# Optimization experiments

Hardware: AMD Instinct MI355X
Metric: run time of the kernel (lower is better)

The kernel has to match this reference:

```python
import jax, jax.numpy as jnp
import numpy as np

B, H, TQ, TK, DH = 4, 8, 128, 128, 64
N_MEM, D_MEM, TOPK, HID = 100000, 512, 32, 128


def setup_inputs() -> dict:
    key = jax.random.key(0)
    ks = jax.random.split(key, 12)
    return {
        "q": jax.random.normal(ks[0], (B, H, TQ, DH), jnp.float32),
        "k_ctx": jax.random.normal(ks[1], (B, H, TK, DH), jnp.float32),
        "v_ctx": jax.random.normal(ks[2], (B, H, TK, DH), jnp.float32),
        "q_for_mem": jax.random.normal(ks[3], (B, TQ, D_MEM), jnp.float32),
        "mem_keys": jax.random.normal(ks[4], (N_MEM, D_MEM), jnp.float32),
        "mem_values": jax.random.normal(ks[5], (N_MEM, D_MEM), jnp.float32),
        "Wk": jax.random.normal(ks[6], (DH, D_MEM), jnp.float32) / np.sqrt(D_MEM),
        "Wv": jax.random.normal(ks[7], (DH, D_MEM), jnp.float32) / np.sqrt(D_MEM),
        "W1": jax.random.normal(ks[8], (HID, 2 * DH), jnp.float32) / np.sqrt(2 * DH),
        "b1": jnp.zeros((HID,), jnp.float32),
        "w2": jax.random.normal(ks[9], (HID,), jnp.float32) / np.sqrt(HID),
        "b2": jnp.zeros((1,), jnp.float32),
    }


def reference(q, k_ctx, v_ctx, q_for_mem, mem_keys, mem_values, Wk, Wv, W1, b1, w2, b2):
    # --- MemoryBank.retrieve: dense scores + top-k gather ---
    mem_scores = jnp.einsum('btd,nd->btn', q_for_mem, mem_keys)          # [B,TQ,N]
    _, idx = jax.lax.top_k(mem_scores, TOPK)                             # [B,TQ,K]
    K_mem = mem_keys[idx] @ Wk.T                                         # [B,TQ,K,DH] (mem_k_proj)
    V_mem = mem_values[idx] @ Wv.T                                       # [B,TQ,K,DH] (mem_v_proj)

    # --- ParametricScoreMLP: f([q;k]) = w2 . relu(W1q q + W1k k + b1) + b2 ---
    W1q, W1k = W1[:, :DH], W1[:, DH:]                                    # split concat linear
    q_part = jnp.einsum('bhtd,ed->bhte', q, W1q)                         # [B,H,TQ,HID]
    kctx_part = jnp.einsum('bhsd,ed->bhse', k_ctx, W1k)                  # [B,H,TK,HID]
    kmem_part = jnp.einsum('btkd,ed->btke', K_mem, W1k)                  # [B,TQ,K,HID]

    h_ctx = jax.nn.relu(q_part[:, :, :, None, :] + kctx_part[:, :, None, :, :] + b1)
    s_ctx = jnp.einsum('bhtse,e->bhts', h_ctx, w2) + b2[0]               # [B,H,TQ,TK]
    h_mem = jax.nn.relu(q_part[:, :, :, None, :] + kmem_part[:, None, :, :, :] + b1)
    s_mem = jnp.einsum('bhtke,e->bhtk', h_mem, w2) + b2[0]               # [B,H,TQ,K]

    scores = jnp.concatenate([s_ctx, s_mem], axis=-1)                    # [B,H,TQ,TK+K]
    weights = jax.nn.softmax(scores, axis=-1)

    w_ctx, w_mem = weights[..., :TK], weights[..., TK:]
    out = jnp.einsum('bhts,bhsd->bhtd', w_ctx, v_ctx) \
        + jnp.einsum('bhtk,btkd->bhtd', w_mem, V_mem)                    # [B,H,TQ,DH]
    return out, weights
```

## Files before the change

kernel.cpp:

```cpp
#include <hip/hip_runtime.h>
#include <cmath>

constexpr int B_ = 4, H_ = 8, TQ_ = 128, TK_ = 128, DH_ = 64;
constexpr int NMEM = 100000, DM = 512, TOPK = 32, HID = 128;
constexpr int R_ = B_ * TQ_;
constexpr int CTILE = 128, RTILE = 64;
constexpr int NCHP = 784;
constexpr int NPAD = NCHP * CTILE;
constexpr int KC = 16;
constexpr int NCAND = NCHP * KC;
constexpr int KSEL = 48;
constexpr int CAP  = 128;
constexpr int NLD  = NCAND / 256;

using f32x4  = __attribute__((ext_vector_type(4))) float;
using bf16x8 = __attribute__((ext_vector_type(8))) short;
using u16x8  = __attribute__((ext_vector_type(8))) unsigned short;

#define GLOAD16(g, l) __builtin_amdgcn_global_load_lds( \
    (const __attribute__((address_space(1))) void*)(g), \
    (__attribute__((address_space(3))) void*)(l), 16, 0, 0)

static __device__ __forceinline__ unsigned short f2bf(float f) {
    unsigned u = __float_as_uint(f);
    u = (u + 0x7FFFu + ((u >> 16) & 1u)) >> 16;
    return (unsigned short)u;
}

__global__ __launch_bounds__(256)
void k0_cvt(const float* __restrict__ mk, const float* __restrict__ qm,
            unsigned short* __restrict__ dst)
{
    const long totalmk = (long)NPAD * DM;
    const long nvalid  = (long)NMEM * DM;
    const long total   = totalmk + (long)R_ * DM;
    long stride = (long)gridDim.x * 256 * 8;
    for (long base = ((long)blockIdx.x * 256 + threadIdx.x) * 8; base < total; base += stride) {
        u16x8 o;
        const float* src = nullptr;
        long off = 0;
        if (base < totalmk) {
            if (base < nvalid) { src = mk; off = base; }
        } else { src = qm; off = base - totalmk; }
        if (src) {
            float4 v0 = *reinterpret_cast<const float4*>(src + off);
            float4 v1 = *reinterpret_cast<const float4*>(src + off + 4);
            o[0] = f2bf(v0.x); o[1] = f2bf(v0.y); o[2] = f2bf(v0.z); o[3] = f2bf(v0.w);
            o[4] = f2bf(v1.x); o[5] = f2bf(v1.y); o[6] = f2bf(v1.z); o[7] = f2bf(v1.w);
        } else {
            o = (u16x8)0;
        }
        *reinterpret_cast<u16x8*>(dst + base) = o;
    }
}

__global__ __launch_bounds__(256)
void k1_mfma(const unsigned short* __restrict__ qmb, const unsigned short* __restrict__ mkb,
             unsigned* __restrict__ cand_k, int* __restrict__ cand_i)
{
    const int wgid = blockIdx.x;
    const int xcd = wgid & 7;
    const int k9 = wgid >> 3;
    const int chunk = xcd * 98 + (k9 >> 3);
    const int rt = k9 & 7;
    const int row0 = rt * RTILE;
    const int col0 = chunk * CTILE;
    const int tid = threadIdx.x;
    const int lane = tid & 63, w = tid >> 6;
    const int wm = w >> 1, wn = w & 1;

    __shared__ __align__(16) char smem[64 * 132 * 4];
    char* Abase = smem;
    char* Bbase = smem + 8192;
    float* scf = (float*)smem;

    const char* srcA[2];
    const char* srcB[4];
#pragma unroll
    for (int p = 0; p < 2; ++p) {
        int X = p * 4096 + w * 1024 + lane * 16;
        int r = X >> 7, c = (X & 127) ^ ((r & 7) << 4);
        srcA[p] = (const char*)qmb + (size_t)(row0 + r) * 1024 + c;
    }
#pragma unroll
    for (int p = 0; p < 4; ++p) {
        int X = p * 4096 + w * 1024 + lane * 16;
        int r = X >> 7, c = (X & 127) ^ ((r & 7) << 4);
        srcB[p] = (const char*)mkb + (size_t)(col0 + r) * 1024 + c;
    }
    int aoff[2][2], boff[4][2];
#pragma unroll
    for (int mi = 0; mi < 2; ++mi) {
        int rr = wm * 32 + mi * 16 + (lane & 15);
        int bse = rr * 128 + ((lane >> 4) * 16);
        aoff[mi][0] = bse ^ ((rr & 7) << 4);
        aoff[mi][1] = (bse + 64) ^ ((rr & 7) << 4);
    }
#pragma unroll
    for (int ni = 0; ni < 4; ++ni) {
        int rr = wn * 64 + ni * 16 + (lane & 15);
        int bse = rr * 128 + ((lane >> 4) * 16);
        boff[ni][0] = 8192 + (bse ^ ((rr & 7) << 4));
        boff[ni][1] = 8192 + ((bse + 64) ^ ((rr & 7) << 4));
    }

    f32x4 acc[2][4];
#pragma unroll
    for (int mi = 0; mi < 2; ++mi)
#pragma unroll
        for (int ni = 0; ni < 4; ++ni) acc[mi][ni] = (f32x4)0.f;

    for (int ks = 0; ks < 8; ++ks) {
#pragma unroll
        for (int p = 0; p < 2; ++p) {
            GLOAD16(srcA[p], Abase + p * 4096 + w * 1024);
            srcA[p] += 128;
        }
#pragma unroll
        for (int p = 0; p < 4; ++p) {
            GLOAD16(srcB[p], Bbase + p * 4096 + w * 1024);
            srcB[p] += 128;
        }
        __syncthreads();
#pragma unroll
        for (int kk = 0; kk < 2; ++kk) {
            bf16x8 af[2], bfr[4];
#pragma unroll
            for (int mi = 0; mi < 2; ++mi)
                af[mi] = *reinterpret_cast<const bf16x8*>(smem + aoff[mi][kk]);
#pragma unroll
            for (int ni = 0; ni < 4; ++ni)
                bfr[ni] = *reinterpret_cast<const bf16x8*>(smem + boff[ni][kk]);
#pragma unroll
            for (int mi = 0; mi < 2; ++mi)
#pragma unroll
                for (int ni = 0; ni < 4; ++ni)
                    acc[mi][ni] = __builtin_amdgcn_mfma_f32_16x16x32_bf16(af[mi], bfr[ni], acc[mi][ni], 0, 0, 0);
        }
        __syncthreads();
    }

#pragma unroll
    for (int mi = 0; mi < 2; ++mi)
#pragma unroll
        for (int ni = 0; ni < 4; ++ni)
#pragma unroll
            for (int reg = 0; reg < 4; ++reg) {
                int rr = wm * 32 + mi * 16 + (lane >> 4) * 4 + reg;
                int cc = wn * 64 + ni * 16 + (lane & 15);
                int pos = ((cc & 31) << 2) | (cc >> 5);
                scf[rr * 132 + pos] = (col0 + cc < NMEM) ? acc[mi][ni][reg] : -INFINITY;
            }
    __syncthreads();

    const int rid = tid >> 2, sub = tid & 3;
    const float* srow = scf + rid * 132 + sub * 32;
    const int bsub = 127 - sub * 8;
    unsigned t0 = 0u, t1 = 0u, t2 = 0u, t3 = 0u;
#pragma unroll
    for (int i = 0; i < 8; ++i) {
        float4 v4 = *reinterpret_cast<const float4*>(srow + i * 4);
        float vv[4] = {v4.x, v4.y, v4.z, v4.w};
#pragma unroll
        for (int q = 0; q < 4; ++q) {
            unsigned b = __float_as_uint(vv[q]);
            unsigned s = b ^ ((unsigned)((int)b >> 31) | 0x80000000u);
            unsigned key = (s & 0xFFFFFF80u) | (unsigned)(bsub - (q * 32 + i));
            bool g0 = key > t0, g1 = key > t1, g2 = key > t2, g3 = key > t3;
            unsigned n0 = g0 ? key : t0;
            unsigned n1 = g0 ? t0 : (g1 ? key : t1);
            unsigned n2 = g1 ? t1 : (g2 ? key : t2);
            unsigned n3 = g2 ? t2 : (g3 ? key : t3);
            t0 = n0; t1 = n1; t2 = n2; t3 = n3;
        }
    }
    size_t base = (size_t)(row0 + rid) * NCAND + (size_t)chunk * KC + sub * 4;
    uint4 kv, iv;
    kv.x = t0; iv.x = col0 + 127 - (int)(t0 & 127u);
    kv.y = t1; iv.y = col0 + 127 - (int)(t1 & 127u);
    kv.z = t2; iv.z = col0 + 127 - (int)(t2 & 127u);
    kv.w = t3; iv.w = col0 + 127 - (int)(t3 & 127u);
    *reinterpret_cast<uint4*>(cand_k + base) = kv;
    *reinterpret_cast<uint4*>(cand_i + base) = iv;
}

__global__ __launch_bounds__(256)
void k2a_thresh(const unsigned* __restrict__ cand_k, const int* __restrict__ cand_i,
                int* __restrict__ cand2_i, int* __restrict__ cand2_n)
{
    const int row = blockIdx.x;
    const int tid = threadIdx.x;
    const int lane = tid & 63, wv = tid >> 6;
    const unsigned* ck = cand_k + (size_t)row * NCAND;

    unsigned key[NLD];
#pragma unroll
    for (int j = 0; j < NLD; ++j) key[j] = ck[tid + j * 256];

    __shared__ int red[4];
    __shared__ int cnt;
    unsigned lo = 0u;
    int c_cur = NCAND;
    for (int bit = 31; bit >= 0; --bit) {
        if (c_cur <= CAP) break;
        unsigned T = lo | (1u << bit);
        int c = 0;
#pragma unroll
        for (int j = 0; j < NLD; ++j) c += (key[j] >= T);
#pragma unroll
        for (int off = 1; off < 64; off <<= 1) c += __shfl_xor(c, off);
        if (lane == 0) red[wv] = c;
        __syncthreads();
        int ct = red[0] + red[1] + red[2] + red[3];
        if (ct >= KSEL) { lo = T; c_cur = ct; }
        __syncthreads();
    }

    if (tid == 0) cnt = 0;
    __syncthreads();
#pragma unroll
    for (int j = 0; j < NLD; ++j) {
        if (key[j] >= lo) {
            int p = atomicAdd(&cnt, 1);
            if (p < CAP) cand2_i[(size_t)row * CAP + p] = cand_i[(size_t)row * NCAND + tid + j * 256];
        }
    }
    __syncthreads();
    if (tid == 0) cand2_n[row] = cnt < CAP ? cnt : CAP;
}

__global__ __launch_bounds__(256)
void k2b_rescore(const float* __restrict__ qm, const float* __restrict__ mk,
                 const int* __restrict__ cand2_i, const int* __restrict__ cand2_n,
                 double* __restrict__ rsc)
{
    const int row = blockIdx.x;
    const int tid = threadIdx.x;
    const int lane = tid & 63, wv = tid >> 6;
    const int c = blockIdx.y * 4 + wv;
    const int n = cand2_n[row];
    if (c >= n) return;
    const int idx = cand2_i[(size_t)row * CAP + c];
    const float4* q4 = reinterpret_cast<const float4*>(qm + (size_t)row * DM);
    const float4* k4 = reinterpret_cast<const float4*>(mk + (size_t)idx * DM);
    float4 a0 = q4[lane], b0 = k4[lane];
    float4 a1 = q4[lane + 64], b1 = k4[lane + 64];
    double p = (double)a0.x * b0.x + (double)a0.y * b0.y
             + (double)a0.z * b0.z + (double)a0.w * b0.w
             + (double)a1.x * b1.x + (double)a1.y * b1.y
             + (double)a1.z * b1.z + (double)a1.w * b1.w;
#pragma unroll
    for (int off = 1; off < 64; off <<= 1) p += __shfl_xor(p, off);
    if (lane == 0) rsc[(size_t)row * CAP + c] = p;
}

__global__ __launch_bounds__(64)
void k2c_top32(const double* __restrict__ rsc, const int* __restrict__ cand2_i,
               const int* __restrict__ cand2_n, int* __restrict__ sel)
{
    const int row = blockIdx.x;
    const int lane = threadIdx.x;
    const int n = cand2_n[row];
    double v0 = -1.0e300, v1 = -1.0e300;
    int i0 = 0x7fffffff, i1 = 0x7fffffff;
    if (lane < n)      { v0 = rsc[(size_t)row * CAP + lane];      i0 = cand2_i[(size_t)row * CAP + lane]; }
    if (lane + 64 < n) { v1 = rsc[(size_t)row * CAP + lane + 64]; i1 = cand2_i[(size_t)row * CAP + lane + 64]; }
    for (int s = 0; s < TOPK; ++s) {
        double bv; int bi;
        if (v0 > v1 || (v0 == v1 && i0 < i1)) { bv = v0; bi = i0; }
        else                                  { bv = v1; bi = i1; }
#pragma unroll
        for (int off = 1; off < 64; off <<= 1) {
            double ov = __shfl_xor(bv, off);
            int    oi = __shfl_xor(bi, off);
            if (ov > bv || (ov == bv && oi < bi)) { bv = ov; bi = oi; }
        }
        if (lane == 0) sel[row * TOPK + s] = bi;
        if (i0 == bi) v0 = -1.0e300;
        if (i1 == bi) v1 = -1.0e300;
    }
}

__global__ __launch_bounds__(128)
void k3_proj(const float* __restrict__ mk, const float* __restrict__ mv,
             const float* __restrict__ Wk, const float* __restrict__ Wv,
             const int* __restrict__ sel,
             float* __restrict__ Kmem, float* __restrict__ Vmem)
{
    const int i0 = blockIdx.x * 8;
    const int tid = threadIdx.x;
    __shared__ float s[2][8][DM];
    __shared__ int si[8];
    if (tid < 8) si[tid] = sel[i0 + tid];
    __syncthreads();
    for (int l = tid; l < 2048; l += 128) {
        int mat = l >> 10, r = (l >> 7) & 7, c4 = l & 127;
        const float* src = (mat ? mv : mk) + (size_t)si[r] * DM + c4 * 4;
        *reinterpret_cast<float4*>(&s[mat][r][c4 * 4]) =
            *reinterpret_cast<const float4*>(src);
    }
    __syncthreads();
    const int doV = tid >> 6;
    const int ep = tid & 63;
    const float* w0 = (doV ? Wv : Wk) + (size_t)ep * DM;
    float a0[8];
#pragma unroll
    for (int r = 0; r < 8; ++r) a0[r] = 0.f;
    for (int d4 = 0; d4 < DM / 4; ++d4) {
        float4 x0 = *reinterpret_cast<const float4*>(w0 + d4 * 4);
#pragma unroll
        for (int r = 0; r < 8; ++r) {
            float4 m = *reinterpret_cast<const float4*>(&s[doV][r][d4 * 4]);
            a0[r] = fmaf(x0.x, m.x, fmaf(x0.y, m.y, fmaf(x0.z, m.z, fmaf(x0.w, m.w, a0[r]))));
        }
    }
    float* O = doV ? Vmem : Kmem;
#pragma unroll
    for (int r = 0; r < 8; ++r)
        O[(size_t)(i0 + r) * DH_ + ep] = a0[r];
}

__global__ __launch_bounds__(128)
void k4_parts(const float* __restrict__ q, const float* __restrict__ kctx,
              const float* __restrict__ Kmem, const float* __restrict__ W1,
              float* __restrict__ qp, float* __restrict__ kcp, float* __restrict__ kmp)
{
    const int bid = blockIdx.x;
    const int tid = threadIdx.x;
    const float* src; float* dst; int woff;
    if (bid < 1024)      { int r0 = bid * 4;          src = q    + (size_t)r0 * DH_; dst = qp  + (size_t)r0 * HID; woff = 0; }
    else if (bid < 2048) { int r0 = (bid - 1024) * 4; src = kctx + (size_t)r0 * DH_; dst = kcp + (size_t)r0 * HID; woff = DH_; }
    else                 { int r0 = (bid - 2048) * 4; src = Kmem + (size_t)r0 * DH_; dst = kmp + (size_t)r0 * HID; woff = DH_; }
    __shared__ float s[4][DH_];
    for (int l = tid; l < 4 * DH_; l += 128) s[l >> 6][l & 63] = src[l];
    __syncthreads();
    const float* wr = W1 + (size_t)tid * (2 * DH_) + woff;
    float a0 = 0.f, a1 = 0.f, a2 = 0.f, a3 = 0.f;
#pragma unroll 8
    for (int d = 0; d < DH_; ++d) {
        float w = wr[d];
        a0 = fmaf(s[0][d], w, a0);
        a1 = fmaf(s[1][d], w, a1);
        a2 = fmaf(s[2][d], w, a2);
        a3 = fmaf(s[3][d], w, a3);
    }
    dst[0 * HID + tid] = a0;
    dst[1 * HID + tid] = a1;
    dst[2 * HID + tid] = a2;
    dst[3 * HID + tid] = a3;
}

__global__ __launch_bounds__(256)
void k5_attn(const float* __restrict__ qp, const float* __restrict__ kcp,
             const float* __restrict__ kmp, const float* __restrict__ vctx,
             const float* __restrict__ Vmem, const float* __restrict__ b1,
             const float* __restrict__ w2, const float* __restrict__ b2,
             float* __restrict__ out, float* __restrict__ outw)
{
    const int bid = blockIdx.x;
    const int t = bid & 127, h = (bid >> 7) & 7, b = bid >> 10;
    const int tid = threadIdx.x;
    const int lane = tid & 63, wv = tid >> 6;
    const int bh = b * H_ + h, bht = bh * TQ_ + t, bt = b * TQ_ + t;
    constexpr int NS = TK_ + TOPK;
    __shared__ float qps[HID], b1s[HID], w2s[HID];
    __shared__ float sc[NS];
    __shared__ float red[8];
    __shared__ float part[4][DH_];
    if (tid < HID) {
        qps[tid] = qp[(size_t)bht * HID + tid];
        b1s[tid] = b1[tid];
        w2s[tid] = w2[tid];
    }
    __syncthreads();
    const float bias2 = b2[0];
    if (tid < NS) {
        const float* kr = (tid < TK_) ? (kcp + ((size_t)bh * TK_ + tid) * HID)
                                      : (kmp + ((size_t)bt * TOPK + (tid - TK_)) * HID);
        float acc = 0.f;
#pragma unroll 4
        for (int e4 = 0; e4 < HID / 4; ++e4) {
            float4 kv = *reinterpret_cast<const float4*>(kr + e4 * 4);
            acc += fmaxf(qps[e4 * 4 + 0] + kv.x + b1s[e4 * 4 + 0], 0.f) * w2s[e4 * 4 + 0];
            acc += fmaxf(qps[e4 * 4 + 1] + kv.y + b1s[e4 * 4 + 1], 0.f) * w2s[e4 * 4 + 1];
            acc += fmaxf(qps[e4 * 4 + 2] + kv.z + b1s[e4 * 4 + 2], 0.f) * w2s[e4 * 4 + 2];
            acc += fmaxf(qps[e4 * 4 + 3] + kv.w + b1s[e4 * 4 + 3], 0.f) * w2s[e4 * 4 + 3];
        }
        sc[tid] = acc + bias2;
    }
    __syncthreads();
    float v = (tid < NS) ? sc[tid] : -INFINITY;
    float m = v;
#pragma unroll
    for (int off = 1; off < 64; off <<= 1) m = fmaxf(m, __shfl_xor(m, off));
    if (lane == 0) red[wv] = m;
    __syncthreads();
    if (tid == 0) red[4] = fmaxf(fmaxf(red[0], red[1]), fmaxf(red[2], red[3]));
    __syncthreads();
    const float mm = red[4];
    float e = (tid < NS) ? expf(v - mm) : 0.f;
    float ssum = e;
#pragma unroll
    for (int off = 1; off < 64; off <<= 1) ssum += __shfl_xor(ssum, off);
    if (lane == 0) red[wv] = ssum;
    __syncthreads();
    if (tid == 0) red[5] = red[0] + red[1] + red[2] + red[3];
    __syncthreads();
    const float inv = 1.f / red[5];
    if (tid < NS) {
        float w = e * inv;
        sc[tid] = w;
        outw[(size_t)bht * NS + tid] = w;
    }
    __syncthreads();
    {
        const int d = lane;
        const int s0 = wv * 40;
        float acc = 0.f;
        for (int s2 = s0; s2 < s0 + 40; ++s2) {
            const float* vrow = (s2 < TK_)
                ? (vctx + ((size_t)bh * TK_ + s2) * DH_)
                : (Vmem + ((size_t)bt * TOPK + (s2 - TK_)) * DH_);
            acc = fmaf(sc[s2], vrow[d], acc);
        }
        part[wv][d] = acc;
    }
    __syncthreads();
    if (tid < DH_)
        out[(size_t)bht * DH_ + tid] = part[0][tid] + part[1][tid] + part[2][tid] + part[3][tid];
}

extern "C" void kernel_launch(void* const* d_in, const int* in_sizes, int n_in,
                              void* d_out, int out_size, void* d_ws, size_t ws_size,
                              hipStream_t stream)
{
    const float* q    = (const float*)d_in[0];
    const float* kctx = (const float*)d_in[1];
    const float* vctx = (const float*)d_in[2];
    const float* qm   = (const float*)d_in[3];
    const float* mk   = (const float*)d_in[4];
    const float* mv   = (const float*)d_in[5];
    const float* Wk   = (const float*)d_in[6];
    const float* Wv   = (const float*)d_in[7];
    const float* W1   = (const float*)d_in[8];
    const float* b1   = (const float*)d_in[9];
    const float* w2   = (const float*)d_in[10];
    const float* b2   = (const float*)d_in[11];
    float* out  = (float*)d_out;
    float* outw = out + (size_t)B_ * H_ * TQ_ * DH_;

    char* w = (char*)d_ws;
    unsigned short* mkb = (unsigned short*)w; w += sizeof(unsigned short) * (size_t)NPAD * DM;
    unsigned short* qmb = (unsigned short*)w; w += sizeof(unsigned short) * R_ * DM;
    unsigned* cand_k = (unsigned*)w; w += sizeof(unsigned) * (size_t)R_ * NCAND;
    int*   cand_i = (int*)w;   w += sizeof(int) * (size_t)R_ * NCAND;
    int*   cand2_i= (int*)w;   w += sizeof(int) * R_ * CAP;
    int*   cand2_n= (int*)w;   w += sizeof(int) * R_;
    double* rsc   = (double*)w; w += sizeof(double) * R_ * CAP;
    int*   sel    = (int*)w;   w += sizeof(int) * R_ * TOPK;
    float* Kmem   = (float*)w; w += sizeof(float) * R_ * TOPK * DH_;
    float* Vmem   = (float*)w; w += sizeof(float) * R_ * TOPK * DH_;
    float* qp     = (float*)w; w += sizeof(float) * B_ * H_ * TQ_ * HID;
    float* kcp    = (float*)w; w += sizeof(float) * B_ * H_ * TK_ * HID;
    float* kmp    = (float*)w; w += sizeof(float) * R_ * TOPK * HID;

    hipLaunchKernelGGL(k0_cvt, dim3(4096), dim3(256), 0, stream, mk, qm, mkb);
    hipLaunchKernelGGL(k1_mfma, dim3(NCHP * 8), dim3(256), 0, stream, qmb, mkb, cand_k, cand_i);
    hipLaunchKernelGGL(k2a_thresh, dim3(R_), dim3(256), 0, stream, cand_k, cand_i, cand2_i, cand2_n);
    hipLaunchKernelGGL(k2b_rescore, dim3(R_, CAP / 4), dim3(256), 0, stream, qm, mk, cand2_i, cand2_n, rsc);
    hipLaunchKernelGGL(k2c_top32, dim3(R_), dim3(64), 0, stream, rsc, cand2_i, cand2_n, sel);
    hipLaunchKernelGGL(k3_proj, dim3(R_ * TOPK / 8), dim3(128), 0, stream, mk, mv, Wk, Wv, sel, Kmem, Vmem);
    hipLaunchKernelGGL(k4_parts, dim3(6144), dim3(128), 0, stream, q, kctx, Kmem, W1, qp, kcp, kmp);
    hipLaunchKernelGGL(k5_attn, dim3(B_ * H_ * TQ_), dim3(256), 0, stream, qp, kcp, kmp, vctx, Vmem, b1, w2, b2, out, outw);
}
```

Baseline: 364.1 us.

## Enlarge score GEMM row tile, derive candidate indices from keys, fuse W1k projection

The memory-score GEMM kernel now processes 128 query rows per block instead of 64. This halves the grid and doubles reuse of each loaded memory-key tile, at the cost of more accumulator registers and a two-pass top-4 epilogue through shared memory. The separate candidate-index array is dropped, and indices are reconstructed in the threshold kernel from the low bits of the packed key, which removes a large global write and read. The W1k projection of retrieved keys is fused into the projection kernel, so the intermediate K_mem buffer and its extra pass in the parts kernel are gone.

```diff
diff --git a/kernel.cpp b/kernel.cpp
--- a/kernel.cpp
+++ b/kernel.cpp
@@ -4,7 +4,7 @@
 constexpr int B_ = 4, H_ = 8, TQ_ = 128, TK_ = 128, DH_ = 64;
 constexpr int NMEM = 100000, DM = 512, TOPK = 32, HID = 128;
 constexpr int R_ = B_ * TQ_;
-constexpr int CTILE = 128, RTILE = 64;
+constexpr int CTILE = 128, RTILE = 128;
 constexpr int NCHP = 784;
 constexpr int NPAD = NCHP * CTILE;
 constexpr int KC = 16;
@@ -56,13 +56,13 @@
 
 __global__ __launch_bounds__(256)
 void k1_mfma(const unsigned short* __restrict__ qmb, const unsigned short* __restrict__ mkb,
-             unsigned* __restrict__ cand_k, int* __restrict__ cand_i)
+             unsigned* __restrict__ cand_k)
 {
     const int wgid = blockIdx.x;
     const int xcd = wgid & 7;
     const int k9 = wgid >> 3;
-    const int chunk = xcd * 98 + (k9 >> 3);
-    const int rt = k9 & 7;
+    const int chunk = xcd * 98 + (k9 >> 2);
+    const int rt = k9 & 3;
     const int row0 = rt * RTILE;
     const int col0 = chunk * CTILE;
     const int tid = threadIdx.x;
@@ -71,27 +71,22 @@
 
     __shared__ __align__(16) char smem[64 * 132 * 4];
     char* Abase = smem;
-    char* Bbase = smem + 8192;
+    char* Bbase = smem + 16384;
     float* scf = (float*)smem;
 
-    const char* srcA[2];
+    const char* srcA[4];
     const char* srcB[4];
 #pragma unroll
-    for (int p = 0; p < 2; ++p) {
+    for (int p = 0; p < 4; ++p) {
         int X = p * 4096 + w * 1024 + lane * 16;
         int r = X >> 7, c = (X & 127) ^ ((r & 7) << 4);
         srcA[p] = (const char*)qmb + (size_t)(row0 + r) * 1024 + c;
-    }
-#pragma unroll
-    for (int p = 0; p < 4; ++p) {
-        int X = p * 4096 + w * 1024 + lane * 16;
-        int r = X >> 7, c = (X & 127) ^ ((r & 7) << 4);
         srcB[p] = (const char*)mkb + (size_t)(col0 + r) * 1024 + c;
     }
-    int aoff[2][2], boff[4][2];
-#pragma unroll
-    for (int mi = 0; mi < 2; ++mi) {
-        int rr = wm * 32 + mi * 16 + (lane & 15);
+    int aoff[4][2], boff[4][2];
+#pragma unroll
+    for (int mi = 0; mi < 4; ++mi) {
+        int rr = wm * 64 + mi * 16 + (lane & 15);
         int bse = rr * 128 + ((lane >> 4) * 16);
         aoff[mi][0] = bse ^ ((rr & 7) << 4);
         aoff[mi][1] = (bse + 64) ^ ((rr & 7) << 4);
@@ -100,39 +95,36 @@
     for (int ni = 0; ni < 4; ++ni) {
         int rr = wn * 64 + ni * 16 + (lane & 15);
         int bse = rr * 128 + ((lane >> 4) * 16);
-        boff[ni][0] = 8192 + (bse ^ ((rr & 7) << 4));
-        boff[ni][1] = 8192 + ((bse + 64) ^ ((rr & 7) << 4));
-    }
-
-    f32x4 acc[2][4];
-#pragma unroll
-    for (int mi = 0; mi < 2; ++mi)
+        boff[ni][0] = 16384 + (bse ^ ((rr & 7) << 4));
+        boff[ni][1] = 16384 + ((bse + 64) ^ ((rr & 7) << 4));
+    }
+
+    f32x4 acc[4][4];
+#pragma unroll
+    for (int mi = 0; mi < 4; ++mi)
 #pragma unroll
         for (int ni = 0; ni < 4; ++ni) acc[mi][ni] = (f32x4)0.f;
 
     for (int ks = 0; ks < 8; ++ks) {
 #pragma unroll
-        for (int p = 0; p < 2; ++p) {
+        for (int p = 0; p < 4; ++p) {
             GLOAD16(srcA[p], Abase + p * 4096 + w * 1024);
             srcA[p] += 128;
-        }
-#pragma unroll
-        for (int p = 0; p < 4; ++p) {
             GLOAD16(srcB[p], Bbase + p * 4096 + w * 1024);
             srcB[p] += 128;
         }
         __syncthreads();
 #pragma unroll
         for (int kk = 0; kk < 2; ++kk) {
-            bf16x8 af[2], bfr[4];
-#pragma unroll
-            for (int mi = 0; mi < 2; ++mi)
+            bf16x8 af[4], bfr[4];
+#pragma unroll
+            for (int mi = 0; mi < 4; ++mi)
                 af[mi] = *reinterpret_cast<const bf16x8*>(smem + aoff[mi][kk]);
 #pragma unroll
             for (int ni = 0; ni < 4; ++ni)
                 bfr[ni] = *reinterpret_cast<const bf16x8*>(smem + boff[ni][kk]);
 #pragma unroll
-            for (int mi = 0; mi < 2; ++mi)
+            for (int mi = 0; mi < 4; ++mi)
 #pragma unroll
                 for (int ni = 0; ni < 4; ++ni)
                     acc[mi][ni] = __builtin_amdgcn_mfma_f32_16x16x32_bf16(af[mi], bfr[ni], acc[mi][ni], 0, 0, 0);
@@ -140,52 +132,52 @@
         __syncthreads();
     }
 
-#pragma unroll
-    for (int mi = 0; mi < 2; ++mi)
-#pragma unroll
-        for (int ni = 0; ni < 4; ++ni)
-#pragma unroll
-            for (int reg = 0; reg < 4; ++reg) {
-                int rr = wm * 32 + mi * 16 + (lane >> 4) * 4 + reg;
-                int cc = wn * 64 + ni * 16 + (lane & 15);
-                int pos = ((cc & 31) << 2) | (cc >> 5);
-                scf[rr * 132 + pos] = (col0 + cc < NMEM) ? acc[mi][ni][reg] : -INFINITY;
+    const int rid = tid >> 2, sub = tid & 3;
+    const int bsub = 127 - sub * 8;
+#pragma unroll
+    for (int h = 0; h < 2; ++h) {
+        if (wm == h) {
+#pragma unroll
+            for (int mi = 0; mi < 4; ++mi)
+#pragma unroll
+                for (int ni = 0; ni < 4; ++ni)
+#pragma unroll
+                    for (int reg = 0; reg < 4; ++reg) {
+                        int rr = mi * 16 + (lane >> 4) * 4 + reg;
+                        int cc = wn * 64 + ni * 16 + (lane & 15);
+                        int pos = ((cc & 31) << 2) | (cc >> 5);
+                        scf[rr * 132 + pos] = (col0 + cc < NMEM) ? acc[mi][ni][reg] : -INFINITY;
+                    }
+        }
+        __syncthreads();
+
+        const float* srow = scf + rid * 132 + sub * 32;
+        unsigned t0 = 0u, t1 = 0u, t2 = 0u, t3 = 0u;
+#pragma unroll
+        for (int i = 0; i < 8; ++i) {
+            float4 v4 = *reinterpret_cast<const float4*>(srow + i * 4);
+            float vv[4] = {v4.x, v4.y, v4.z, v4.w};
+#pragma unroll
+            for (int q = 0; q < 4; ++q) {
+                unsigned b = __float_as_uint(vv[q]);
+                unsigned s = b ^ ((unsigned)((int)b >> 31) | 0x80000000u);
+                unsigned key = (s & 0xFFFFFF80u) | (unsigned)(bsub - (q * 32 + i));
+                bool g0 = key > t0, g1 = key > t1, g2 = key > t2, g3 = key > t3;
+                unsigned n0 = g0 ? key : t0;
+                unsigned n1 = g0 ? t0 : (g1 ? key : t1);
+                unsigned n2 = g1 ? t1 : (g2 ? key : t2);
+                unsigned n3 = g2 ? t2 : (g3 ? key : t3);
+                t0 = n0; t1 = n1; t2 = n2; t3 = n3;
             }
-    __syncthreads();
-
-    const int rid = tid >> 2, sub = tid & 3;
-    const float* srow = scf + rid * 132 + sub * 32;
-    const int bsub = 127 - sub * 8;
-    unsigned t0 = 0u, t1 = 0u, t2 = 0u, t3 = 0u;
-#pragma unroll
-    for (int i = 0; i < 8; ++i) {
-        float4 v4 = *reinterpret_cast<const float4*>(srow + i * 4);
-        float vv[4] = {v4.x, v4.y, v4.z, v4.w};
-#pragma unroll
-        for (int q = 0; q < 4; ++q) {
-            unsigned b = __float_as_uint(vv[q]);
-            unsigned s = b ^ ((unsigned)((int)b >> 31) | 0x80000000u);
-            unsigned key = (s & 0xFFFFFF80u) | (unsigned)(bsub - (q * 32 + i));
-            bool g0 = key > t0, g1 = key > t1, g2 = key > t2, g3 = key > t3;
-            unsigned n0 = g0 ? key : t0;
-            unsigned n1 = g0 ? t0 : (g1 ? key : t1);
-            unsigned n2 = g1 ? t1 : (g2 ? key : t2);
-            unsigned n3 = g2 ? t2 : (g3 ? key : t3);
-            t0 = n0; t1 = n1; t2 = n2; t3 = n3;
-        }
-    }
-    size_t base = (size_t)(row0 + rid) * NCAND + (size_t)chunk * KC + sub * 4;
-    uint4 kv, iv;
-    kv.x = t0; iv.x = col0 + 127 - (int)(t0 & 127u);
-    kv.y = t1; iv.y = col0 + 127 - (int)(t1 & 127u);
-    kv.z = t2; iv.z = col0 + 127 - (int)(t2 & 127u);
-    kv.w = t3; iv.w = col0 + 127 - (int)(t3 & 127u);
-    *reinterpret_cast<uint4*>(cand_k + base) = kv;
-    *reinterpret_cast<uint4*>(cand_i + base) = iv;
+        }
+        size_t base = (size_t)(row0 + h * 64 + rid) * NCAND + (size_t)chunk * KC + sub * 4;
+        *reinterpret_cast<uint4*>(cand_k + base) = make_uint4(t0, t1, t2, t3);
+        __syncthreads();
+    }
 }
 
 __global__ __launch_bounds__(256)
-void k2a_thresh(const unsigned* __restrict__ cand_k, const int* __restrict__ cand_i,
+void k2a_thresh(const unsigned* __restrict__ cand_k,
                 int* __restrict__ cand2_i, int* __restrict__ cand2_n)
 {
     const int row = blockIdx.x;
@@ -222,7 +214,12 @@
     for (int j = 0; j < NLD; ++j) {
         if (key[j] >= lo) {
             int p = atomicAdd(&cnt, 1);
-            if (p < CAP) cand2_i[(size_t)row * CAP + p] = cand_i[(size_t)row * NCAND + tid + j * 256];
+            if (p < CAP) {
+                int ipos = tid + j * 256;
+                int chunk = ipos >> 4;
+                int col = (chunk << 7) + 127 - (int)(key[j] & 127u);
+                cand2_i[(size_t)row * CAP + p] = col;
+            }
         }
     }
     __syncthreads();
@@ -284,12 +281,13 @@
 __global__ __launch_bounds__(128)
 void k3_proj(const float* __restrict__ mk, const float* __restrict__ mv,
              const float* __restrict__ Wk, const float* __restrict__ Wv,
-             const int* __restrict__ sel,
-             float* __restrict__ Kmem, float* __restrict__ Vmem)
+             const float* __restrict__ W1, const int* __restrict__ sel,
+             float* __restrict__ kmp, float* __restrict__ Vmem)
 {
     const int i0 = blockIdx.x * 8;
     const int tid = threadIdx.x;
     __shared__ float s[2][8][DM];
+    __shared__ float sKm[8][DH_];
     __shared__ int si[8];
     if (tid < 8) si[tid] = sel[i0 + tid];
     __syncthreads();
@@ -314,23 +312,42 @@
             a0[r] = fmaf(x0.x, m.x, fmaf(x0.y, m.y, fmaf(x0.z, m.z, fmaf(x0.w, m.w, a0[r]))));
         }
     }
-    float* O = doV ? Vmem : Kmem;
+    if (doV) {
+#pragma unroll
+        for (int r = 0; r < 8; ++r)
+            Vmem[(size_t)(i0 + r) * DH_ + ep] = a0[r];
+    } else {
+#pragma unroll
+        for (int r = 0; r < 8; ++r)
+            sKm[r][ep] = a0[r];
+    }
+    __syncthreads();
+    const float* wr = W1 + (size_t)tid * (2 * DH_) + DH_;
+    float acc[8];
+#pragma unroll
+    for (int r = 0; r < 8; ++r) acc[r] = 0.f;
+#pragma unroll 8
+    for (int d = 0; d < DH_; ++d) {
+        float wv2 = wr[d];
+#pragma unroll
+        for (int r = 0; r < 8; ++r)
+            acc[r] = fmaf(sKm[r][d], wv2, acc[r]);
+    }
 #pragma unroll
     for (int r = 0; r < 8; ++r)
-        O[(size_t)(i0 + r) * DH_ + ep] = a0[r];
+        kmp[(size_t)(i0 + r) * HID + tid] = acc[r];
 }
 
 __global__ __launch_bounds__(128)
 void k4_parts(const float* __restrict__ q, const float* __restrict__ kctx,
-              const float* __restrict__ Kmem, const float* __restrict__ W1,
-              float* __restrict__ qp, float* __restrict__ kcp, float* __restrict__ kmp)
+              const float* __restrict__ W1,
+              float* __restrict__ qp, float* __restrict__ kcp)
 {
     const int bid = blockIdx.x;
     const int tid = threadIdx.x;
     const float* src; float* dst; int woff;
     if (bid < 1024)      { int r0 = bid * 4;          src = q    + (size_t)r0 * DH_; dst = qp  + (size_t)r0 * HID; woff = 0; }
-    else if (bid < 2048) { int r0 = (bid - 1024) * 4; src = kctx + (size_t)r0 * DH_; dst = kcp + (size_t)r0 * HID; woff = DH_; }
-    else                 { int r0 = (bid - 2048) * 4; src = Kmem + (size_t)r0 * DH_; dst = kmp + (size_t)r0 * HID; woff = DH_; }
+    else                 { int r0 = (bid - 1024) * 4; src = kctx + (size_t)r0 * DH_; dst = kcp + (size_t)r0 * HID; woff = DH_; }
     __shared__ float s[4][DH_];
     for (int l = tid; l < 4 * DH_; l += 128) s[l >> 6][l & 63] = src[l];
     __syncthreads();
@@ -453,23 +470,21 @@
     unsigned short* mkb = (unsigned short*)w; w += sizeof(unsigned short) * (size_t)NPAD * DM;
     unsigned short* qmb = (unsigned short*)w; w += sizeof(unsigned short) * R_ * DM;
     unsigned* cand_k = (unsigned*)w; w += sizeof(unsigned) * (size_t)R_ * NCAND;
-    int*   cand_i = (int*)w;   w += sizeof(int) * (size_t)R_ * NCAND;
     int*   cand2_i= (int*)w;   w += sizeof(int) * R_ * CAP;
     int*   cand2_n= (int*)w;   w += sizeof(int) * R_;
     double* rsc   = (double*)w; w += sizeof(double) * R_ * CAP;
     int*   sel    = (int*)w;   w += sizeof(int) * R_ * TOPK;
-    float* Kmem   = (float*)w; w += sizeof(float) * R_ * TOPK * DH_;
     float* Vmem   = (float*)w; w += sizeof(float) * R_ * TOPK * DH_;
     float* qp     = (float*)w; w += sizeof(float) * B_ * H_ * TQ_ * HID;
     float* kcp    = (float*)w; w += sizeof(float) * B_ * H_ * TK_ * HID;
     float* kmp    = (float*)w; w += sizeof(float) * R_ * TOPK * HID;
 
     hipLaunchKernelGGL(k0_cvt, dim3(4096), dim3(256), 0, stream, mk, qm, mkb);
-    hipLaunchKernelGGL(k1_mfma, dim3(NCHP * 8), dim3(256), 0, stream, qmb, mkb, cand_k, cand_i);
-    hipLaunchKernelGGL(k2a_thresh, dim3(R_), dim3(256), 0, stream, cand_k, cand_i, cand2_i, cand2_n);
+    hipLaunchKernelGGL(k1_mfma, dim3(NCHP * 4), dim3(256), 0, stream, qmb, mkb, cand_k);
+    hipLaunchKernelGGL(k2a_thresh, dim3(R_), dim3(256), 0, stream, cand_k, cand2_i, cand2_n);
     hipLaunchKernelGGL(k2b_rescore, dim3(R_, CAP / 4), dim3(256), 0, stream, qm, mk, cand2_i, cand2_n, rsc);
     hipLaunchKernelGGL(k2c_top32, dim3(R_), dim3(64), 0, stream, rsc, cand2_i, cand2_n, sel);
-    hipLaunchKernelGGL(k3_proj, dim3(R_ * TOPK / 8), dim3(128), 0, stream, mk, mv, Wk, Wv, sel, Kmem, Vmem);
-    hipLaunchKernelGGL(k4_parts, dim3(6144), dim3(128), 0, stream, q, kctx, Kmem, W1, qp, kcp, kmp);
+    hipLaunchKernelGGL(k3_proj, dim3(R_ * TOPK / 8), dim3(128), 0, stream, mk, mv, Wk, Wv, W1, sel, kmp, Vmem);
+    hipLaunchKernelGGL(k4_parts, dim3(2048), dim3(128), 0, stream, q, kctx, W1, qp, kcp);
     hipLaunchKernelGGL(k5_attn, dim3(B_ * H_ * TQ_), dim3(256), 0, stream, qp, kcp, kmp, vctx, Vmem, b1, w2, b2, out, outw);
 }
```

Measured after the change: 361.9 us. About the same (-0.6%).
